# Kernel optimization log

Measured on AMD Instinct MI355X. Metric: run time of the kernel, lower is better.

The kernel has to match this reference:

```python
import jax, jax.numpy as jnp
import numpy as np

B, L, P, NH = 16384, 64, 2, 128
T = L // P          # number of patches (GRU steps)
NOUT = 1 << P       # softmax over 2**p possible patches


def setup_inputs() -> dict:
    key = jax.random.key(0)
    ks = jax.random.split(key, 10)
    s_in = 1.0 / np.sqrt(NH)
    x = jax.random.randint(ks[0], (B, L, 1), 0, 2).astype(jnp.float32)
    return {
        "x": x,
        # GRU params, torch layout: gates ordered (r, z, n)
        "w_ih": jax.random.normal(ks[1], (3 * NH, P), jnp.float32) * s_in,
        "w_hh": jax.random.normal(ks[2], (3 * NH, NH), jnp.float32) * s_in,
        "b_ih": jax.random.normal(ks[3], (3 * NH,), jnp.float32) * s_in,
        "b_hh": jax.random.normal(ks[4], (3 * NH,), jnp.float32) * s_in,
        # MLP head: Linear(Nh,Nh) -> ReLU -> Linear(Nh, 2**p) -> Softmax
        "w1": jax.random.normal(ks[5], (NH, NH), jnp.float32) * s_in,
        "b1": jax.random.normal(ks[6], (NH,), jnp.float32) * s_in,
        "w2": jax.random.normal(ks[7], (NOUT, NH), jnp.float32) * s_in,
        "b2": jax.random.normal(ks[8], (NOUT,), jnp.float32) * s_in,
    }


def _gru_mlp_logp(x, w_ih, w_hh, b_ih, b_hh, w1, b1, w2, b2):
    b = x.shape[0]
    patches = x.reshape(b, T, P)                       # Patch1D.forward
    # shift right by one patch (teacher forcing input), first step is zeros
    data = jnp.concatenate([jnp.zeros((b, 1, P), x.dtype), patches[:, :-1]], axis=1)
    # precompute all input-side gate projections: [B,T,3*Nh]
    xi = jnp.einsum('btp,gp->btg', data, w_ih) + b_ih

    def step(h, xi_t):
        gi_r, gi_z, gi_n = jnp.split(xi_t, 3, axis=-1)
        gh = h @ w_hh.T + b_hh
        gh_r, gh_z, gh_n = jnp.split(gh, 3, axis=-1)
        r = jax.nn.sigmoid(gi_r + gh_r)
        z = jax.nn.sigmoid(gi_z + gh_z)
        n = jnp.tanh(gi_n + r * gh_n)
        h_new = (1.0 - z) * n + z * h
        return h_new, h_new

    h0 = jnp.zeros((b, NH), x.dtype)
    _, hs = jax.lax.scan(step, h0, jnp.swapaxes(xi, 0, 1))  # [T,B,Nh]
    hs = jnp.swapaxes(hs, 0, 1)                              # [B,T,Nh]

    hid = jax.nn.relu(hs @ w1.T + b1)
    probs = jax.nn.softmax(hid @ w2.T + b2, axis=-1)         # [B,T,2**p]

    # genpatch2onehot: binary-encode each patch, little-endian (bit i -> 2**i)
    weights = (1 << jnp.arange(P)).astype(jnp.float32)
    idx = jnp.sum(patches * weights, axis=-1).astype(jnp.int32)  # [B,T]
    total = jnp.take_along_axis(probs, idx[..., None], axis=-1)[..., 0]
    return jnp.sum(jnp.log(total), axis=1)                   # [B]


def reference(x, w_ih, w_hh, b_ih, b_hh, w1, b1, w2, b2):
    return _gru_mlp_logp(x, w_ih, w_hh, b_ih, b_hh, w1, b1, w2, b2)
```

## Files before the change

kernel.cpp:

```cpp
#include <hip/hip_runtime.h>
#include <hip/hip_bf16.h>


#define NSTEP 32
#define BT    16
#define BLK   512

using s8v = __attribute__((ext_vector_type(8))) short;
using f4v = __attribute__((ext_vector_type(4))) float;

#define L2E 1.4426950408889634f
#define LN2 0.6931471805599453f

__device__ __forceinline__ unsigned short f2bf(float f) {
  __hip_bfloat16 h = __float2bfloat16(f);
  return __builtin_bit_cast(unsigned short, h);
}
__device__ __forceinline__ unsigned pkbf2(float a, float b) {
  return (unsigned)f2bf(a) | ((unsigned)f2bf(b) << 16);
}
__device__ __forceinline__ s8v pack8s(float sc, float4 u, float4 v) {
  s8v a;
  a[0]=(short)f2bf(sc*u.x); a[1]=(short)f2bf(sc*u.y); a[2]=(short)f2bf(sc*u.z); a[3]=(short)f2bf(sc*u.w);
  a[4]=(short)f2bf(sc*v.x); a[5]=(short)f2bf(sc*v.y); a[6]=(short)f2bf(sc*v.z); a[7]=(short)f2bf(sc*v.w);
  return a;
}
__device__ __forceinline__ f4v mfma16(s8v a, s8v b, f4v c) {
  return __builtin_amdgcn_mfma_f32_16x16x32_bf16(a, b, c, 0, 0, 0);
}
__device__ __forceinline__ float sigm2(float x) {
  return __builtin_amdgcn_rcpf(1.f + __builtin_amdgcn_exp2f(-x));
}
__device__ __forceinline__ float tanh2(float x) {
  return __builtin_fmaf(2.f, __builtin_amdgcn_rcpf(1.f + __builtin_amdgcn_exp2f(-x)), -1.f);
}

__global__ void prep_kernel(const float* __restrict__ w1, const float* __restrict__ w2,
                            unsigned char* __restrict__ ws) {
  const int task = blockIdx.x;
  const int l = threadIdx.x;
  if (task < 32) {
    const int mt = task >> 2, ks = task & 3;
    const float* src = w1 + (16*mt + (l & 15)) * 128 + ks*32 + (l >> 4)*8;
    *(s8v*)(ws + (task*64 + l)*16) = pack8s(1.f, *(const float4*)src, *(const float4*)(src + 4));
  } else {
    const int ks = task - 32;
    s8v fr;
    #pragma unroll
    for (int e = 0; e < 8; ++e) fr[e] = (short)0;
    if ((l & 15) < 4) {
      const float* src = w2 + (l & 15) * 128 + ks*32 + (l >> 4)*8;
      fr = pack8s(1.f, *(const float4*)src, *(const float4*)(src + 4));
    }
    *(s8v*)(ws + 32768 + (ks*64 + l)*16) = fr;
  }
}

__global__ __launch_bounds__(BLK, 4) void prnn_kernel(
    const float* __restrict__ x, const float* __restrict__ w_ih,
    const float* __restrict__ w_hh, const float* __restrict__ b_ih,
    const float* __restrict__ b_hh, const float* __restrict__ b1,
    const float* __restrict__ b2, const unsigned char* __restrict__ ws,
    float* __restrict__ out) {

  __shared__ __align__(16) unsigned char lds_h[4*64*16];
  __shared__ __align__(16) unsigned char lds_hid[4*64*16];
  __shared__ __align__(16) float lds_xrz[64*4*4];
  __shared__ __align__(16) float lds_xn[32*4*4];
  __shared__ __align__(16) float lds_bb[256];
  __shared__ __align__(16) float lds_b2[4];
  __shared__ unsigned lds_idx[16*8];
  __shared__ float lds_lp[8][16];

  const int tid = threadIdx.x;
  const int bbase = blockIdx.x * BT;
  const int lane = tid & 63;
  const int lg = lane >> 4, ln = lane & 15;
  const int w = __builtin_amdgcn_readfirstlane(tid >> 6);

  if (tid < 128) {
    int b = tid >> 3, ch = tid & 7;
    const float* xp = x + (size_t)(bbase + b) * 64 + ch * 8;
    float4 v0 = *(const float4*)xp, v1 = *(const float4*)(xp + 4);
    unsigned pk = ((v0.x!=0.f?1u:0u) | (v0.y!=0.f?2u:0u))
               | (((v0.z!=0.f?1u:0u) | (v0.w!=0.f?2u:0u)) << 8)
               | (((v1.x!=0.f?1u:0u) | (v1.y!=0.f?2u:0u)) << 16)
               | (((v1.z!=0.f?1u:0u) | (v1.w!=0.f?2u:0u)) << 24);
    lds_idx[b*8 + ch] = pk;
  }
  if (tid < 256) {
    int j = tid;
    float base = b_ih[j] + b_hh[j];
    float wa = w_ih[2*j], wb = w_ih[2*j+1];
    int qq = j >> 2, e = j & 3;
    #pragma unroll
    for (int v = 0; v < 4; ++v)
      lds_xrz[(qq*4+v)*4 + e] = L2E * (base + ((v&1) ? wa : 0.f) + ((v&2) ? wb : 0.f));
  }
  if (tid < 128) {
    int j2 = 256 + tid;
    float bn = b_ih[j2];
    float wan = w_ih[2*j2], wbn = w_ih[2*j2+1];
    int qn = tid >> 2, en = tid & 3;
    #pragma unroll
    for (int v = 0; v < 4; ++v)
      lds_xn[(qn*4+v)*4 + en] = (2.f*L2E) * (bn + ((v&1) ? wan : 0.f) + ((v&2) ? wbn : 0.f));
  }
  if (tid < 128) lds_bb[tid] = (2.f*L2E) * b_hh[256 + tid];
  else if (tid < 256) lds_bb[tid] = b1[tid - 128];
  if (tid < 4) lds_b2[tid] = b2[tid];

  s8v Ar[4], Az[4], An[4];
  {
    const int row = 16*w + ln;
    #pragma unroll
    for (int ks = 0; ks < 4; ++ks) {
      const float* s0 = w_hh + row*128 + ks*32 + lg*8;
      Ar[ks] = pack8s(L2E, *(const float4*)s0, *(const float4*)(s0 + 4));
      const float* s1 = s0 + 128*128;
      Az[ks] = pack8s(L2E, *(const float4*)s1, *(const float4*)(s1 + 4));
      const float* s2 = s0 + 256*128;
      An[ks] = pack8s(2.f*L2E, *(const float4*)s2, *(const float4*)(s2 + 4));
    }
  }
  const int q = 4*w + lg;
  const s8v* __restrict__ wsf = (const s8v*)ws;

  __syncthreads();

  unsigned pk0a = 0, pk0b = 0;
  #pragma unroll
  for (int w8 = 0; w8 < 4; ++w8) {
    unsigned u = lds_idx[ln*8 + w8];
    pk0a |= (((u&3u) | ((u>>6)&0xCu) | ((u>>12)&0x30u) | ((u>>18)&0xC0u)) << (8*w8));
    unsigned u2 = lds_idx[ln*8 + 4 + w8];
    pk0b |= (((u2&3u) | ((u2>>6)&0xCu) | ((u2>>12)&0x30u) | ((u2>>18)&0xC0u)) << (8*w8));
  }

  const unsigned wroff =
      (unsigned)((((w>>1)*64 + 16*(2*(w&1) + (lg>>1)) + ln)*16) + 8*(lg&1));

  s8v Bf[4];
  #pragma unroll
  for (int ks = 0; ks < 4; ++ks)
    #pragma unroll
    for (int e = 0; e < 8; ++e) Bf[ks][e] = (short)0;
  f4v hfr;
  hfr[0]=0.f; hfr[1]=0.f; hfr[2]=0.f; hfr[3]=0.f;
  float lp0 = 0.f;
  int pv0 = 0;

  for (int tb = 0; tb < NSTEP; tb += 8) {
    const unsigned pc0 = (tb & 16) ? pk0b : pk0a;
    #pragma unroll
    for (int k = 0; k < 8; ++k) {
      const int t = tb + k;
      {
        const int var = pv0;
        f4v aR = *(const f4v*)&lds_xrz[(q*4 + var)*4];
        f4v aZ = *(const f4v*)&lds_xrz[((q+32)*4 + var)*4];
        f4v aN = *(const f4v*)&lds_bb[q*4];
        #pragma unroll
        for (int ks = 0; ks < 4; ++ks) {
          aR = mfma16(Ar[ks], Bf[ks], aR);
          aZ = mfma16(Az[ks], Bf[ks], aZ);
          aN = mfma16(An[ks], Bf[ks], aN);
        }
        const f4v xnv = *(const f4v*)&lds_xn[(q*4 + var)*4];
        f4v hn;
        #pragma unroll
        for (int r = 0; r < 4; ++r) {
          float R  = sigm2(aR[r]);
          float Z  = sigm2(aZ[r]);
          float Ng = tanh2(__builtin_fmaf(R, aN[r], xnv[r]));
          hn[r] = __builtin_fmaf(Z, hfr[r] - Ng, Ng);
        }
        hfr = hn;
        uint2 wv;
        wv.x = pkbf2(hn[0], hn[1]);
        wv.y = pkbf2(hn[2], hn[3]);
        *(uint2*)(&lds_h[wroff]) = wv;
      }
      __syncthreads();
      #pragma unroll
      for (int ks = 0; ks < 4; ++ks)
        Bf[ks] = *(const s8v*)(&lds_h[(ks*64 + lane)*16]);
      {
        f4v hc = *(const f4v*)&lds_bb[128 + q*4];
        #pragma unroll
        for (int ks = 0; ks < 4; ++ks)
          hc = mfma16(wsf[(w*4 + ks)*64 + lane], Bf[ks], hc);
        uint2 wv;
        wv.x = pkbf2(fmaxf(hc[0],0.f), fmaxf(hc[1],0.f));
        wv.y = pkbf2(fmaxf(hc[2],0.f), fmaxf(hc[3],0.f));
        *(uint2*)(&lds_hid[wroff]) = wv;
      }
      __syncthreads();
      const int ic0 = (int)((pc0 >> ((2*t) & 31)) & 3);
      if (w == k) {
        f4v la;
        if (lg == 0) la = *(const f4v*)lds_b2;
        else { la[0]=0.f; la[1]=0.f; la[2]=0.f; la[3]=0.f; }
        #pragma unroll
        for (int ks = 0; ks < 4; ++ks)
          la = mfma16(wsf[2048 + ks*64 + lane],
                      *(const s8v*)(&lds_hid[(ks*64 + lane)*16]), la);
        if (lg == 0) {
          const int ic = (int)(((t & 16) ? pk0b : pk0a) >> ((2*t) & 31)) & 3;
          float l0=la[0], l1=la[1], l2=la[2], l3=la[3];
          float m = fmaxf(fmaxf(l0, l1), fmaxf(l2, l3));
          float s = __builtin_amdgcn_exp2f((l0-m)*L2E) + __builtin_amdgcn_exp2f((l1-m)*L2E)
                  + __builtin_amdgcn_exp2f((l2-m)*L2E) + __builtin_amdgcn_exp2f((l3-m)*L2E);
          float sel = (ic == 0) ? l0 : (ic == 1) ? l1 : (ic == 2) ? l2 : l3;
          lp0 += (sel - m) - __builtin_amdgcn_logf(s) * LN2;
        }
      }
      pv0 = ic0;
    }
  }

  if (lg == 0) lds_lp[w][ln] = lp0;
  __syncthreads();
  if (tid < 16) {
    float s = 0.f;
    #pragma unroll
    for (int ww = 0; ww < 8; ++ww) s += lds_lp[ww][tid];
    out[bbase + tid] = s;
  }
}

extern "C" void kernel_launch(void* const* d_in, const int* in_sizes, int n_in,
                              void* d_out, int out_size, void* d_ws, size_t ws_size,
                              hipStream_t stream) {
  const float* x    = (const float*)d_in[0];
  const float* w_ih = (const float*)d_in[1];
  const float* w_hh = (const float*)d_in[2];
  const float* b_ih = (const float*)d_in[3];
  const float* b_hh = (const float*)d_in[4];
  const float* w1   = (const float*)d_in[5];
  const float* b1   = (const float*)d_in[6];
  const float* w2   = (const float*)d_in[7];
  const float* b2   = (const float*)d_in[8];
  float* out = (float*)d_out;
  unsigned char* ws = (unsigned char*)d_ws;

  prep_kernel<<<36, 64, 0, stream>>>(w1, w2, ws);

  int B = in_sizes[0] / 64;
  int grid = B / BT;
  prnn_kernel<<<grid, BLK, 0, stream>>>(x, w_ih, w_hh, b_ih, b_hh, b1, b2, ws, out);
}
```

Baseline: 111.8 us.

## Double-buffer LDS hidden states to drop one barrier per GRU step

The hidden-state and MLP-hidden LDS buffers are double-buffered by step parity. The output-head softmax for step t-1 is deferred into step t. This removes the second __syncthreads per step, so the head computation of one wave overlaps the next step's recurrence. The 8-way unrolled loop becomes an unroll-1 loop, which may lose some scheduling freedom, and LDS use doubles for these buffers, which could affect occupancy.

```diff
diff --git a/kernel.cpp b/kernel.cpp
--- a/kernel.cpp
+++ b/kernel.cpp
@@ -63,8 +63,8 @@
     const float* __restrict__ b2, const unsigned char* __restrict__ ws,
     float* __restrict__ out) {
 
-  __shared__ __align__(16) unsigned char lds_h[4*64*16];
-  __shared__ __align__(16) unsigned char lds_hid[4*64*16];
+  __shared__ __align__(16) unsigned char lds_h[2][4*64*16];
+  __shared__ __align__(16) unsigned char lds_hid[2][4*64*16];
   __shared__ __align__(16) float lds_xrz[64*4*4];
   __shared__ __align__(16) float lds_xn[32*4*4];
   __shared__ __align__(16) float lds_bb[256];
@@ -150,74 +150,76 @@
   float lp0 = 0.f;
   int pv0 = 0;
 
-  for (int tb = 0; tb < NSTEP; tb += 8) {
-    const unsigned pc0 = (tb & 16) ? pk0b : pk0a;
-    #pragma unroll
-    for (int k = 0; k < 8; ++k) {
-      const int t = tb + k;
-      {
-        const int var = pv0;
-        f4v aR = *(const f4v*)&lds_xrz[(q*4 + var)*4];
-        f4v aZ = *(const f4v*)&lds_xrz[((q+32)*4 + var)*4];
-        f4v aN = *(const f4v*)&lds_bb[q*4];
-        #pragma unroll
-        for (int ks = 0; ks < 4; ++ks) {
-          aR = mfma16(Ar[ks], Bf[ks], aR);
-          aZ = mfma16(Az[ks], Bf[ks], aZ);
-          aN = mfma16(An[ks], Bf[ks], aN);
-        }
-        const f4v xnv = *(const f4v*)&lds_xn[(q*4 + var)*4];
-        f4v hn;
-        #pragma unroll
-        for (int r = 0; r < 4; ++r) {
-          float R  = sigm2(aR[r]);
-          float Z  = sigm2(aZ[r]);
-          float Ng = tanh2(__builtin_fmaf(R, aN[r], xnv[r]));
-          hn[r] = __builtin_fmaf(Z, hfr[r] - Ng, Ng);
-        }
-        hfr = hn;
-        uint2 wv;
-        wv.x = pkbf2(hn[0], hn[1]);
-        wv.y = pkbf2(hn[2], hn[3]);
-        *(uint2*)(&lds_h[wroff]) = wv;
+  auto do_p5 = [&](int u, int uslot) {
+    if (w == (u & 7)) {
+      f4v la;
+      if (lg == 0) la = *(const f4v*)lds_b2;
+      else { la[0]=0.f; la[1]=0.f; la[2]=0.f; la[3]=0.f; }
+      #pragma unroll
+      for (int ks = 0; ks < 4; ++ks)
+        la = mfma16(wsf[2048 + ks*64 + lane],
+                    *(const s8v*)(&lds_hid[uslot][(ks*64 + lane)*16]), la);
+      if (lg == 0) {
+        const int ic = (int)((((u & 16) ? pk0b : pk0a) >> ((2*u) & 31)) & 3);
+        float l0=la[0], l1=la[1], l2=la[2], l3=la[3];
+        float m = fmaxf(fmaxf(l0, l1), fmaxf(l2, l3));
+        float s = __builtin_amdgcn_exp2f((l0-m)*L2E) + __builtin_amdgcn_exp2f((l1-m)*L2E)
+                + __builtin_amdgcn_exp2f((l2-m)*L2E) + __builtin_amdgcn_exp2f((l3-m)*L2E);
+        float sel = (ic == 0) ? l0 : (ic == 1) ? l1 : (ic == 2) ? l2 : l3;
+        lp0 += (sel - m) - __builtin_amdgcn_logf(s) * LN2;
       }
-      __syncthreads();
+    }
+  };
+
+  #pragma unroll 1
+  for (int t = 0; t < NSTEP; ++t) {
+    const int slot = t & 1;
+    {
+      const int var = pv0;
+      f4v aR = *(const f4v*)&lds_xrz[(q*4 + var)*4];
+      f4v aZ = *(const f4v*)&lds_xrz[((q+32)*4 + var)*4];
+      f4v aN = *(const f4v*)&lds_bb[q*4];
+      #pragma unroll
+      for (int ks = 0; ks < 4; ++ks) {
+        aR = mfma16(Ar[ks], Bf[ks], aR);
+        aZ = mfma16(Az[ks], Bf[ks], aZ);
+        aN = mfma16(An[ks], Bf[ks], aN);
+      }
+      const f4v xnv = *(const f4v*)&lds_xn[(q*4 + var)*4];
+      f4v hn;
+      #pragma unroll
+      for (int r = 0; r < 4; ++r) {
+        float R  = sigm2(aR[r]);
+        float Z  = sigm2(aZ[r]);
+        float Ng = tanh2(__builtin_fmaf(R, aN[r], xnv[r]));
+        hn[r] = __builtin_fmaf(Z, hfr[r] - Ng, Ng);
+      }
+      hfr = hn;
+      uint2 wv;
+      wv.x = pkbf2(hn[0], hn[1]);
+      wv.y = pkbf2(hn[2], hn[3]);
+      *(uint2*)(&lds_h[slot][wroff]) = wv;
+    }
+    __syncthreads();
+    #pragma unroll
+    for (int ks = 0; ks < 4; ++ks)
+      Bf[ks] = *(const s8v*)(&lds_h[slot][(ks*64 + lane)*16]);
+    {
+      f4v hc = *(const f4v*)&lds_bb[128 + q*4];
       #pragma unroll
       for (int ks = 0; ks < 4; ++ks)
-        Bf[ks] = *(const s8v*)(&lds_h[(ks*64 + lane)*16]);
-      {
-        f4v hc = *(const f4v*)&lds_bb[128 + q*4];
-        #pragma unroll
-        for (int ks = 0; ks < 4; ++ks)
-          hc = mfma16(wsf[(w*4 + ks)*64 + lane], Bf[ks], hc);
-        uint2 wv;
-        wv.x = pkbf2(fmaxf(hc[0],0.f), fmaxf(hc[1],0.f));
-        wv.y = pkbf2(fmaxf(hc[2],0.f), fmaxf(hc[3],0.f));
-        *(uint2*)(&lds_hid[wroff]) = wv;
-      }
-      __syncthreads();
-      const int ic0 = (int)((pc0 >> ((2*t) & 31)) & 3);
-      if (w == k) {
-        f4v la;
-        if (lg == 0) la = *(const f4v*)lds_b2;
-        else { la[0]=0.f; la[1]=0.f; la[2]=0.f; la[3]=0.f; }
-        #pragma unroll
-        for (int ks = 0; ks < 4; ++ks)
-          la = mfma16(wsf[2048 + ks*64 + lane],
-                      *(const s8v*)(&lds_hid[(ks*64 + lane)*16]), la);
-        if (lg == 0) {
-          const int ic = (int)(((t & 16) ? pk0b : pk0a) >> ((2*t) & 31)) & 3;
-          float l0=la[0], l1=la[1], l2=la[2], l3=la[3];
-          float m = fmaxf(fmaxf(l0, l1), fmaxf(l2, l3));
-          float s = __builtin_amdgcn_exp2f((l0-m)*L2E) + __builtin_amdgcn_exp2f((l1-m)*L2E)
-                  + __builtin_amdgcn_exp2f((l2-m)*L2E) + __builtin_amdgcn_exp2f((l3-m)*L2E);
-          float sel = (ic == 0) ? l0 : (ic == 1) ? l1 : (ic == 2) ? l2 : l3;
-          lp0 += (sel - m) - __builtin_amdgcn_logf(s) * LN2;
-        }
-      }
-      pv0 = ic0;
-    }
-  }
+        hc = mfma16(wsf[(w*4 + ks)*64 + lane], Bf[ks], hc);
+      uint2 wv;
+      wv.x = pkbf2(fmaxf(hc[0],0.f), fmaxf(hc[1],0.f));
+      wv.y = pkbf2(fmaxf(hc[2],0.f), fmaxf(hc[3],0.f));
+      *(uint2*)(&lds_hid[slot][wroff]) = wv;
+    }
+    if (t > 0) do_p5(t - 1, slot ^ 1);
+    pv0 = (int)((((t & 16) ? pk0b : pk0a) >> ((2*t) & 31)) & 3);
+  }
+
+  __syncthreads();
+  do_p5(NSTEP - 1, (NSTEP - 1) & 1);
 
   if (lg == 0) lds_lp[w][ln] = lp0;
   __syncthreads();
```

Result: no change. 110.0 us (-1.6%).
